# Kernel tuning notes

Measured on AMD Instinct MI355X. Metric: run time of the kernel, lower is better.

The kernel has to match this reference:

```python
import jax, jax.numpy as jnp
import numpy as np

N, H, C = 1024, 128, 7

def _linear_params(key, din, dout):
    k1, k2 = jax.random.split(key)
    bound = 1.0 / np.sqrt(din)
    W = jax.random.uniform(k1, (din, dout), minval=-bound, maxval=bound, dtype=jnp.float32)
    b = jax.random.uniform(k2, (dout,), minval=-bound, maxval=bound, dtype=jnp.float32)
    return W, b

def setup_inputs() -> dict:
    key = jax.random.key(0)
    ks = jax.random.split(key, 6)
    e = jax.random.normal(ks[0], (N, H), dtype=jnp.float32)
    c = jax.random.uniform(ks[1], (N, N, C), dtype=jnp.float32)
    mW1, mb1 = _linear_params(ks[2], 2 * H + C, H)
    mW2, mb2 = _linear_params(ks[3], H, H)
    uW1, ub1 = _linear_params(ks[4], 2 * H, H)
    uW2, ub2 = _linear_params(ks[5], H, H)
    return {"e": e, "c": c,
            "mW1": mW1, "mb1": mb1, "mW2": mW2, "mb2": mb2,
            "uW1": uW1, "ub1": ub1, "uW2": uW2, "ub2": ub2}

def reference(e, c, mW1, mb1, mW2, mb2, uW1, ub1, uW2, ub2):
    n = e.shape[0]
    # z[i,j] = concat(e[i], e[j], c[i,j])  -> [N, N, 2H+C]
    x = jnp.broadcast_to(e[:, None, :], (n, n, H))  # sender rows
    y = jnp.broadcast_to(e[None, :, :], (n, n, H))  # receiver cols
    z = jnp.concatenate([x, y, c], axis=2)
    h = jax.nn.relu(jnp.einsum('ijk,kh->ijh', z, mW1) + mb1)
    m = jnp.einsum('ijh,hk->ijk', h, mW2) + mb2
    agg = m.sum(axis=1)  # [N, H]
    u = jnp.concatenate([agg, e], axis=1)  # [N, 2H]
    out = jax.nn.relu(u @ uW1 + ub1) @ uW2 + ub2
    return out
```

## Files before the change

### kernel.cpp

```cpp
#include <hip/hip_runtime.h>

#define NN 1024
#define HH 128
#define CC 7
#define BI 8
#define BJ 64
#define NCH 4
#define NSLICE 16
#define QPAD 132

typedef __attribute__((ext_vector_type(8))) short bf16x8;
typedef __attribute__((ext_vector_type(4))) float f32x4;

__device__ inline unsigned short f2bf(float x) {
    union { float f; unsigned u; } v; v.f = x;
    unsigned u = v.u + 0x7FFFu + ((v.u >> 16) & 1);
    return (unsigned short)(u >> 16);
}
__device__ inline unsigned bfrnd(unsigned u) {
    return u + 0x7FFFu + ((u >> 16) & 1u);
}

__global__ __launch_bounds__(256) void precompute_pq(
    const float* __restrict__ e, const float* __restrict__ mW1,
    const float* __restrict__ mb1, float* __restrict__ P, float* __restrict__ Q)
{
    const int t  = threadIdx.x;
    const int rr = t >> 7;
    const int h  = t & 127;
    const int i0 = blockIdx.x * 2;
    __shared__ float eL[2][HH];
    eL[rr][h] = e[(size_t)(i0 + rr) * HH + h];
    __syncthreads();
    float p = mb1[h], q = 0.f;
    for (int k = 0; k < HH; ++k) {
        const float ev = eL[rr][k];
        p = fmaf(ev, mW1[k * HH + h], p);
        q = fmaf(ev, mW1[(HH + k) * HH + h], q);
    }
    P[(size_t)(i0 + rr) * HH + h] = p;
    Q[(size_t)(i0 + rr) * HH + h] = q;
}

__global__ __launch_bounds__(256, 3) void msg_mfma(
    const float* __restrict__ c, const float* __restrict__ mW1,
    const float* __restrict__ P, const float* __restrict__ Q,
    float* __restrict__ HSp)
{
    const int bid   = blockIdx.x;
    const int islab = bid >> 4;
    const int slice = bid & 15;
    const int i0    = islab * BI;
    const int j0b   = slice * BJ;
    const int t     = threadIdx.x;
    const int w     = t >> 6;
    const int l     = t & 63;
    const int g     = l >> 4;
    const int col   = l & 15;
    const int iw0   = i0 + 2 * w;

    __shared__ float qch[BJ * QPAD];
    __shared__ uint4 abuf[BI * BJ];

    #pragma unroll
    for (int rep = 0; rep < 8; ++rep) {
        const int f4  = t + rep * 256;
        const int row = f4 >> 5;
        const int c4  = (f4 & 31) * 4;
        *(f32x4*)(qch + row * QPAD + c4) =
            *(const f32x4*)(Q + (size_t)(j0b + row) * HH + c4);
    }
    #pragma unroll
    for (int rep = 0; rep < 2; ++rep) {
        const int rr = t + rep * 256;
        const int ii = rr >> 6;
        const int jj = rr & 63;
        const unsigned* __restrict__ cp = (const unsigned*)
            (c + ((size_t)(i0 + ii) * NN + j0b + jj) * CC);
        unsigned d0 = bfrnd(cp[0]), d1 = bfrnd(cp[1]), d2 = bfrnd(cp[2]);
        unsigned d3 = bfrnd(cp[3]), d4 = bfrnd(cp[4]), d5 = bfrnd(cp[5]);
        unsigned d6 = bfrnd(cp[6]);
        uint4 pk;
        pk.x = __builtin_amdgcn_perm(d1, d0, 0x07060302u);
        pk.y = __builtin_amdgcn_perm(d3, d2, 0x07060302u);
        pk.z = __builtin_amdgcn_perm(d5, d4, 0x07060302u);
        pk.w = d6 >> 16;
        abuf[rr] = pk;
    }

    bf16x8 bfr[8];
    #pragma unroll
    for (int ht = 0; ht < 8; ++ht) {
        bf16x8 bv = {0,0,0,0,0,0,0,0};
        if (g == 0) {
            #pragma unroll
            for (int k = 0; k < CC; ++k)
                ((short*)&bv)[k] = (short)f2bf(mW1[(2 * HH + k) * HH + 16 * ht + col]);
        }
        bfr[ht] = bv;
    }
    float pv[2][8];
    #pragma unroll
    for (int ii = 0; ii < 2; ++ii)
        #pragma unroll
        for (int ht = 0; ht < 8; ++ht)
            pv[ii][ht] = P[(size_t)(iw0 + ii) * HH + 16 * ht + col];

    float acc[2][8];
    #pragma unroll
    for (int ii = 0; ii < 2; ++ii)
        #pragma unroll
        for (int ht = 0; ht < 8; ++ht) acc[ii][ht] = 0.f;

    __syncthreads();

    for (int ch = 0; ch < NCH; ++ch) {
        const uint4 a0 = abuf[(2 * w + 0) * 64 + ch * 16 + col];
        const uint4 a1 = abuf[(2 * w + 1) * 64 + ch * 16 + col];
        const bf16x8 af0 = __builtin_bit_cast(bf16x8, a0);
        const bf16x8 af1 = __builtin_bit_cast(bf16x8, a1);
        const int qbase = (ch * 16 + g * 4) * QPAD + col;
        #pragma unroll
        for (int ht = 0; ht < 8; ++ht) {
            f32x4 d0, d1;
            #pragma unroll
            for (int r = 0; r < 4; ++r) {
                const float q = qch[qbase + r * QPAD + 16 * ht];
                d0[r] = pv[0][ht] + q;
                d1[r] = pv[1][ht] + q;
            }
            d0 = __builtin_amdgcn_mfma_f32_16x16x32_bf16(af0, bfr[ht], d0, 0, 0, 0);
            d1 = __builtin_amdgcn_mfma_f32_16x16x32_bf16(af1, bfr[ht], d1, 0, 0, 0);
            #pragma unroll
            for (int r = 0; r < 4; ++r) {
                acc[0][ht] += fmaxf(d0[r], 0.f);
                acc[1][ht] += fmaxf(d1[r], 0.f);
            }
        }
    }

    #pragma unroll
    for (int ii = 0; ii < 2; ++ii)
        #pragma unroll
        for (int ht = 0; ht < 8; ++ht) {
            float a = acc[ii][ht];
            a += __shfl_xor(a, 16, 64);
            a += __shfl_xor(a, 32, 64);
            acc[ii][ht] = a;
        }
    #pragma unroll
    for (int ii = 0; ii < 2; ++ii)
        #pragma unroll
        for (int s = 0; s < 2; ++s) {
            const int ht = g + 4 * s;
            HSp[((size_t)slice * NN + iw0 + ii) * HH + 16 * ht + col] = acc[ii][ht];
        }
}

__global__ __launch_bounds__(256) void final_mlp(
    const float* __restrict__ e, const float* __restrict__ HSp,
    const float* __restrict__ mW2, const float* __restrict__ mb2,
    const float* __restrict__ uW1, const float* __restrict__ ub1,
    const float* __restrict__ uW2, const float* __restrict__ ub2,
    float* __restrict__ out)
{
    const int t  = threadIdx.x;
    const int s  = t >> 7;
    const int h  = t & 127;
    const int i0 = blockIdx.x * 2;
    __shared__ float hsL[2][HH], eL[2][HH], aggL[2][HH], t1L[2][HH], part[2][2][HH];

    {
        const size_t ih = (size_t)(i0 + s) * HH + h;
        float sum = 0.f;
        #pragma unroll
        for (int sl = 0; sl < NSLICE; ++sl)
            sum += HSp[(size_t)sl * NN * HH + ih];
        hsL[s][h] = sum;
        eL[s][h]  = e[ih];
    }
    __syncthreads();

    {
        float a0 = 0.f, a1 = 0.f;
        const int k0 = 64 * s;
        for (int k = k0; k < k0 + 64; ++k) {
            const float wv = mW2[k * HH + h];
            a0 = fmaf(hsL[0][k], wv, a0);
            a1 = fmaf(hsL[1][k], wv, a1);
        }
        part[s][0][h] = a0; part[s][1][h] = a1;
    }
    __syncthreads();
    aggL[s][h] = part[0][s][h] + part[1][s][h] + (float)NN * mb2[h];
    __syncthreads();

    {
        float b0 = 0.f, b1 = 0.f;
        const float* __restrict__ src   = (s == 0) ? &aggL[0][0] : &eL[0][0];
        const float* __restrict__ wbase = uW1 + (size_t)s * HH * HH;
        for (int k = 0; k < HH; ++k) {
            const float wv = wbase[k * HH + h];
            b0 = fmaf(src[k],      wv, b0);
            b1 = fmaf(src[HH + k], wv, b1);
        }
        part[s][0][h] = b0; part[s][1][h] = b1;
    }
    __syncthreads();
    t1L[s][h] = fmaxf(part[0][s][h] + part[1][s][h] + ub1[h], 0.f);
    __syncthreads();

    {
        float c0 = 0.f, c1 = 0.f;
        const int k0 = 64 * s;
        for (int k = k0; k < k0 + 64; ++k) {
            const float wv = uW2[k * HH + h];
            c0 = fmaf(t1L[0][k], wv, c0);
            c1 = fmaf(t1L[1][k], wv, c1);
        }
        part[s][0][h] = c0; part[s][1][h] = c1;
    }
    __syncthreads();
    out[(size_t)(i0 + s) * HH + h] = part[0][s][h] + part[1][s][h] + ub2[h];
}

extern "C" void kernel_launch(void* const* d_in, const int* in_sizes, int n_in,
                              void* d_out, int out_size, void* d_ws, size_t ws_size,
                              hipStream_t stream) {
    const float* e   = (const float*)d_in[0];
    const float* c   = (const float*)d_in[1];
    const float* mW1 = (const float*)d_in[2];
    const float* mb1 = (const float*)d_in[3];
    const float* mW2 = (const float*)d_in[4];
    const float* mb2 = (const float*)d_in[5];
    const float* uW1 = (const float*)d_in[6];
    const float* ub1 = (const float*)d_in[7];
    const float* uW2 = (const float*)d_in[8];
    const float* ub2 = (const float*)d_in[9];
    float* out = (float*)d_out;

    float* P   = (float*)d_ws;
    float* Q   = P + NN * HH;
    float* HSp = Q + NN * HH;

    precompute_pq<<<NN / 2, 256, 0, stream>>>(e, mW1, mb1, P, Q);
    msg_mfma<<<(NN / BI) * NSLICE, 256, 0, stream>>>(c, mW1, P, Q, HSp);
    final_mlp<<<NN / 2, 256, 0, stream>>>(e, HSp, mW2, mb2, uW1, ub1, uW2, ub2, out);
}
```

Baseline: 50.89 us.

## Store Q as packed bf16 pairs to halve LDS footprint and raise occupancy

Q is now rounded to bf16 in precompute_pq, and columns h and h+64 are packed into one 32-bit word. The message kernel stages half as much shared memory per block, reads one word per pair of hidden tiles and unpacks it with shifts. Launch bounds go from 3 to 4 blocks per CU, and the block index mapping swaps so consecutive blocks cover different i-slabs of the same j-slice, which shares Q tiles in cache. The trade-off is extra rounding of Q to bf16, which lowers accuracy, plus a few unpack ALU ops.

```diff
diff --git a/kernel.cpp b/kernel.cpp
--- a/kernel.cpp
+++ b/kernel.cpp
@@ -7,29 +7,32 @@
 #define BJ 64
 #define NCH 4
 #define NSLICE 16
-#define QPAD 132
+#define QPADU 68
 
 typedef __attribute__((ext_vector_type(8))) short bf16x8;
 typedef __attribute__((ext_vector_type(4))) float f32x4;
 
-__device__ inline unsigned short f2bf(float x) {
+__device__ inline unsigned f2bf(float x) {
     union { float f; unsigned u; } v; v.f = x;
-    unsigned u = v.u + 0x7FFFu + ((v.u >> 16) & 1);
-    return (unsigned short)(u >> 16);
+    return (v.u + 0x7FFFu + ((v.u >> 16) & 1u)) >> 16;
 }
 __device__ inline unsigned bfrnd(unsigned u) {
     return u + 0x7FFFu + ((u >> 16) & 1u);
 }
+__device__ inline float bitsf(unsigned u) {
+    union { unsigned u; float f; } v; v.u = u; return v.f;
+}
 
 __global__ __launch_bounds__(256) void precompute_pq(
     const float* __restrict__ e, const float* __restrict__ mW1,
-    const float* __restrict__ mb1, float* __restrict__ P, float* __restrict__ Q)
+    const float* __restrict__ mb1, float* __restrict__ P, unsigned* __restrict__ Qpk)
 {
     const int t  = threadIdx.x;
     const int rr = t >> 7;
     const int h  = t & 127;
     const int i0 = blockIdx.x * 2;
     __shared__ float eL[2][HH];
+    __shared__ float qs[2][HH];
     eL[rr][h] = e[(size_t)(i0 + rr) * HH + h];
     __syncthreads();
     float p = mb1[h], q = 0.f;
@@ -39,17 +42,23 @@
         q = fmaf(ev, mW1[(HH + k) * HH + h], q);
     }
     P[(size_t)(i0 + rr) * HH + h] = p;
-    Q[(size_t)(i0 + rr) * HH + h] = q;
-}
-
-__global__ __launch_bounds__(256, 3) void msg_mfma(
+    qs[rr][h] = q;
+    __syncthreads();
+    if (h < 64) {
+        const unsigned lo = f2bf(qs[rr][h]);
+        const unsigned hi = f2bf(qs[rr][h + 64]);
+        Qpk[(size_t)(i0 + rr) * 64 + h] = lo | (hi << 16);
+    }
+}
+
+__global__ __launch_bounds__(256, 4) void msg_mfma(
     const float* __restrict__ c, const float* __restrict__ mW1,
-    const float* __restrict__ P, const float* __restrict__ Q,
+    const float* __restrict__ P, const unsigned* __restrict__ Qpk,
     float* __restrict__ HSp)
 {
     const int bid   = blockIdx.x;
-    const int islab = bid >> 4;
-    const int slice = bid & 15;
+    const int islab = bid & 127;
+    const int slice = bid >> 7;
     const int i0    = islab * BI;
     const int j0b   = slice * BJ;
     const int t     = threadIdx.x;
@@ -59,16 +68,16 @@
     const int col   = l & 15;
     const int iw0   = i0 + 2 * w;
 
-    __shared__ float qch[BJ * QPAD];
+    __shared__ unsigned qpk[BJ * QPADU];
     __shared__ uint4 abuf[BI * BJ];
 
     #pragma unroll
-    for (int rep = 0; rep < 8; ++rep) {
-        const int f4  = t + rep * 256;
-        const int row = f4 >> 5;
-        const int c4  = (f4 & 31) * 4;
-        *(f32x4*)(qch + row * QPAD + c4) =
-            *(const f32x4*)(Q + (size_t)(j0b + row) * HH + c4);
+    for (int rep = 0; rep < 4; ++rep) {
+        const int idx = t + rep * 256;
+        const int row = idx >> 4;
+        const int c4  = (idx & 15) * 4;
+        *(uint4*)(qpk + row * QPADU + c4) =
+            *(const uint4*)(Qpk + (size_t)(j0b + row) * 64 + c4);
     }
     #pragma unroll
     for (int rep = 0; rep < 2; ++rep) {
@@ -115,26 +124,37 @@
     __syncthreads();
 
     for (int ch = 0; ch < NCH; ++ch) {
-        const uint4 a0 = abuf[(2 * w + 0) * 64 + ch * 16 + col];
-        const uint4 a1 = abuf[(2 * w + 1) * 64 + ch * 16 + col];
-        const bf16x8 af0 = __builtin_bit_cast(bf16x8, a0);
-        const bf16x8 af1 = __builtin_bit_cast(bf16x8, a1);
-        const int qbase = (ch * 16 + g * 4) * QPAD + col;
-        #pragma unroll
-        for (int ht = 0; ht < 8; ++ht) {
-            f32x4 d0, d1;
+        const bf16x8 af0 = __builtin_bit_cast(bf16x8, abuf[(2 * w + 0) * 64 + ch * 16 + col]);
+        const bf16x8 af1 = __builtin_bit_cast(bf16x8, abuf[(2 * w + 1) * 64 + ch * 16 + col]);
+        unsigned qd[4][4];
+        #pragma unroll
+        for (int r = 0; r < 4; ++r) {
+            const unsigned* __restrict__ qr =
+                qpk + (ch * 16 + g * 4 + r) * QPADU + col;
+            #pragma unroll
+            for (int hp = 0; hp < 4; ++hp) qd[r][hp] = qr[16 * hp];
+        }
+        #pragma unroll
+        for (int hp = 0; hp < 4; ++hp) {
+            f32x4 dA0, dA1, dB0, dB1;
             #pragma unroll
             for (int r = 0; r < 4; ++r) {
-                const float q = qch[qbase + r * QPAD + 16 * ht];
-                d0[r] = pv[0][ht] + q;
-                d1[r] = pv[1][ht] + q;
+                const unsigned u = qd[r][hp];
+                const float fa = bitsf(u << 16);
+                const float fb = bitsf(u & 0xFFFF0000u);
+                dA0[r] = pv[0][hp] + fa;     dA1[r] = pv[1][hp] + fa;
+                dB0[r] = pv[0][hp + 4] + fb; dB1[r] = pv[1][hp + 4] + fb;
             }
-            d0 = __builtin_amdgcn_mfma_f32_16x16x32_bf16(af0, bfr[ht], d0, 0, 0, 0);
-            d1 = __builtin_amdgcn_mfma_f32_16x16x32_bf16(af1, bfr[ht], d1, 0, 0, 0);
+            dA0 = __builtin_amdgcn_mfma_f32_16x16x32_bf16(af0, bfr[hp],     dA0, 0, 0, 0);
+            dA1 = __builtin_amdgcn_mfma_f32_16x16x32_bf16(af1, bfr[hp],     dA1, 0, 0, 0);
+            dB0 = __builtin_amdgcn_mfma_f32_16x16x32_bf16(af0, bfr[hp + 4], dB0, 0, 0, 0);
+            dB1 = __builtin_amdgcn_mfma_f32_16x16x32_bf16(af1, bfr[hp + 4], dB1, 0, 0, 0);
             #pragma unroll
             for (int r = 0; r < 4; ++r) {
-                acc[0][ht] += fmaxf(d0[r], 0.f);
-                acc[1][ht] += fmaxf(d1[r], 0.f);
+                acc[0][hp]     += fmaxf(dA0[r], 0.f);
+                acc[1][hp]     += fmaxf(dA1[r], 0.f);
+                acc[0][hp + 4] += fmaxf(dB0[r], 0.f);
+                acc[1][hp + 4] += fmaxf(dB1[r], 0.f);
             }
         }
     }
@@ -239,11 +259,11 @@
     const float* ub2 = (const float*)d_in[9];
     float* out = (float*)d_out;
 
-    float* P   = (float*)d_ws;
-    float* Q   = P + NN * HH;
-    float* HSp = Q + NN * HH;
-
-    precompute_pq<<<NN / 2, 256, 0, stream>>>(e, mW1, mb1, P, Q);
-    msg_mfma<<<(NN / BI) * NSLICE, 256, 0, stream>>>(c, mW1, P, Q, HSp);
+    float*    P   = (float*)d_ws;
+    unsigned* Qpk = (unsigned*)(P + NN * HH);
+    float*    HSp = (float*)(Qpk + NN * 64);
+
+    precompute_pq<<<NN / 2, 256, 0, stream>>>(e, mW1, mb1, P, Qpk);
+    msg_mfma<<<(NN / BI) * NSLICE, 256, 0, stream>>>(c, mW1, P, Qpk, HSp);
     final_mlp<<<NN / 2, 256, 0, stream>>>(e, HSp, mW2, mb2, uW1, ub1, uW2, ub2, out);
 }
```

After: 187.3 us. +268.0%, slower.
